# Kernel tuning notes

Hardware: AMD Instinct MI355X
Metric: run time of the kernel (lower is better)

Reference implementation:

```python
import jax, jax.numpy as jnp
import numpy as np
import math

S, B, D_MODEL = 1024, 2, 1024
N_HEADS = 16
D_HEAD = D_MODEL // N_HEADS
C = 32  # compressed_len


def _xavier(key, shape):
    fan_in, fan_out = shape[-1], shape[-2] if len(shape) > 1 else shape[-1]
    limit = math.sqrt(6.0 / (fan_in + fan_out))
    return jax.random.uniform(key, shape, jnp.float32, -limit, limit)


def setup_inputs() -> dict:
    key = jax.random.key(0)
    ks = jax.random.split(key, 10)
    return {
        "x": jax.random.normal(ks[0], (S, B, D_MODEL), jnp.float32),
        "q_down": _xavier(ks[1], (C, D_MODEL)),
        "Wq": _xavier(ks[2], (D_MODEL, D_MODEL)),
        "bq": jnp.zeros((D_MODEL,), jnp.float32),
        "Wk": _xavier(ks[3], (D_MODEL, D_MODEL)),
        "bk": jnp.zeros((D_MODEL,), jnp.float32),
        "Wv": _xavier(ks[4], (D_MODEL, D_MODEL)),
        "bv": jnp.zeros((D_MODEL,), jnp.float32),
        "Wo": _xavier(ks[5], (D_MODEL, D_MODEL)),
        "bo": jnp.zeros((D_MODEL,), jnp.float32),
    }


def reference(x, q_down, Wq, bq, Wk, bk, Wv, bv, Wo, bo):
    # x: (s, b, d_model); causal=True, rope=None, dropout inactive (eval)
    s, b, d_model = x.shape
    h, dh = N_HEADS, D_HEAD
    scale = 1.0 / math.sqrt(dh)

    q_u = x @ Wq.T + bq                       # (s,b,dm)
    k_d = x @ Wk.T + bk
    v_d = x @ Wv.T + bv
    v_d_k = v_d @ Wk.T + bk
    v_d_v = v_d @ Wv.T + bv

    def heads(t):  # (s,b,dm) -> (b,h,s,dh)
        return t.reshape(s, b, h, dh).transpose(1, 2, 0, 3)

    q_u = heads(q_u) * scale
    k_d = heads(k_d)
    v_d_kv = jnp.concatenate([heads(v_d_k), heads(v_d_v)], axis=-1)  # (b,h,s,2dh)

    q_d = q_down.reshape(C, h, dh).transpose(1, 0, 2) * scale        # (h,c,dh)

    down = jnp.einsum('hcd,bhsd->bhcs', q_d, k_d)                    # (b,h,c,s)
    w = jnp.exp(down - jnp.max(down, axis=-1, keepdims=True))
    norm = jnp.cumsum(w, axis=-1)

    # (b,h,c,s,2dh): running compressed KV state
    kv_u = jnp.cumsum(w[..., None] * v_d_kv[:, :, None, :, :], axis=3) / norm[..., None]
    k_u, v_u = jnp.split(kv_u, 2, axis=-1)                           # each (b,h,c,s,dh)

    up = jnp.einsum('bhsd,bhcsd->bhsc', q_u, k_u)
    up = jax.nn.softmax(up, axis=-1)
    out = jnp.einsum('bhsc,bhcsd->bhsd', up, v_u)                    # (b,h,s,dh)

    out = out.transpose(2, 0, 1, 3).reshape(s, b, d_model)
    return out @ Wo.T + bo
```

## Files before the change

kernel.cpp:

```cpp
#include <hip/hip_runtime.h>
#include <cstdint>
#include <cstddef>

#define S_LEN 1024
#define BATCH 2
#define DM    1024
#define NH    16
#define DH    64
#define CC    32
#define SB    2048
#define TSD   128
#define NCHD  8

using short8 = __attribute__((ext_vector_type(8))) short;
using f32x4  = __attribute__((ext_vector_type(4))) float;

__device__ __forceinline__ float b2f(unsigned short u) {
    union { unsigned int i; float f; } v; v.i = ((unsigned int)u) << 16; return v.f;
}
__device__ __forceinline__ unsigned short f2b(float f) {
    union { float f; unsigned int i; } v; v.f = f;
    unsigned int x = v.i;
    unsigned int r = x + 0x7FFFu + ((x >> 16) & 1u);
    return (unsigned short)(r >> 16);
}

__device__ __forceinline__ void async_ld16(const unsigned short* g, unsigned short* l) {
    __builtin_amdgcn_global_load_lds(
        (const __attribute__((address_space(1))) unsigned int*)g,
        (__attribute__((address_space(3))) unsigned int*)l,
        16, 0, 0);
}

__global__ __launch_bounds__(256) void k_convert(
    const void* x, const void* qd,
    const void* wq, const void* wk, const void* wv, const void* wo,
    const void* bq, const void* bk, const void* bv, const void* bo,
    int* __restrict__ flag,
    unsigned short* xb, unsigned short* qdb,
    unsigned short* Wqb, unsigned short* Wkb, unsigned short* Wvb, unsigned short* Wob,
    float* biasf)
{
    __shared__ int cnt;
    if (threadIdx.x == 0) cnt = 0;
    __syncthreads();
    {
        const unsigned short* xs = (const unsigned short*)x;
        int local = 0;
        for (int i = threadIdx.x; i < 1024; i += 256) {
            unsigned e = (xs[i * 2] >> 7) & 0xFF;
            if (e >= 90 && e <= 160) local++;
        }
        atomicAdd(&cnt, local);
    }
    __syncthreads();
    const int isbf = (cnt >= 640);
    if (blockIdx.x == 0 && threadIdx.x == 0) *flag = isbf;

    const size_t tid = (size_t)blockIdx.x * 256 + threadIdx.x;
    const size_t stride = (size_t)gridDim.x * 256;

    if (!isbf) {
        auto cv = [&](const void* src, unsigned short* dst, size_t n) {
            const float4* s = (const float4*)src;
            for (size_t i = tid; i < n / 4; i += stride) {
                float4 v = s[i];
                ushort4 o;
                o.x = f2b(v.x); o.y = f2b(v.y); o.z = f2b(v.z); o.w = f2b(v.w);
                ((ushort4*)dst)[i] = o;
            }
        };
        cv(x,  xb,  (size_t)SB * DM);
        cv(qd, qdb, (size_t)CC * DM);
        cv(wq, Wqb, (size_t)DM * DM);
        cv(wk, Wkb, (size_t)DM * DM);
        cv(wv, Wvb, (size_t)DM * DM);
        cv(wo, Wob, (size_t)DM * DM);
    }
    for (size_t i = tid; i < 5 * DM; i += stride) {
        int w = (int)(i >> 10), o = (int)(i & 1023);
        float val;
        if (w == 4) val = 0.f;
        else {
            const void* bp = (w == 0) ? bq : ((w == 1) ? bk : ((w == 2) ? bv : bo));
            val = isbf ? b2f(((const unsigned short*)bp)[o]) : ((const float*)bp)[o];
        }
        biasf[i] = val;
    }
}

__global__ __launch_bounds__(256) void k_prep(const unsigned short* __restrict__ Wv0,
                                              const unsigned short* __restrict__ Wv1,
                                              const unsigned short* __restrict__ Wk0,
                                              const unsigned short* __restrict__ Wk1,
                                              const int* __restrict__ flag,
                                              const float* __restrict__ biasf,
                                              unsigned short* __restrict__ WvT,
                                              float* __restrict__ b2k,
                                              float* __restrict__ b2v)
{
    const int isbf = *flag;
    const unsigned short* Wvb = isbf ? Wv1 : Wv0;
    const unsigned short* Wkb = isbf ? Wk1 : Wk0;
    const int t = threadIdx.x;
    if (blockIdx.x < 128) {
        const int r0 = (blockIdx.x & 7) * 128;
        const int c0 = (blockIdx.x >> 3) * 64;
        __shared__ unsigned short T[128 * 68];
        for (int u = t; u < 128 * 8; u += 256) {
            int r = u >> 3, cb = (u & 7) * 8;
            *(short8*)&T[r * 68 + cb] = *(const short8*)&Wvb[(size_t)(r0 + r) * DM + c0 + cb];
        }
        __syncthreads();
        for (int u = t; u < 64 * 16; u += 256) {
            int c = u >> 4, r8 = (u & 15) * 8;
            short8 o;
#pragma unroll
            for (int k = 0; k < 8; ++k) o[k] = T[(r8 + k) * 68 + c];
            *(short8*)&WvT[(size_t)(c0 + c) * DM + r0 + r8] = o;
        }
    } else {
        const int idx = blockIdx.x - 128;
        const int set = idx >> 5;
        const int bx = idx & 31;
        const unsigned short* W = set ? Wvb : Wkb;
        const float* bvf = biasf + 2048;
        const float* badd = set ? (biasf + 2048) : (biasf + 1024);
        float* out = set ? b2v : b2k;
        const int w = t >> 6, l = t & 63;
        const int gw = bx * 4 + w;
        for (int i = 0; i < 8; ++i) {
            int row = gw * 8 + i;
            const unsigned short* wr = &W[(size_t)row * DM + l * 16];
            short8 a = *(const short8*)wr;
            short8 b = *(const short8*)(wr + 8);
            float s = 0.f;
#pragma unroll
            for (int j = 0; j < 8; ++j) {
                s += b2f((unsigned short)a[j]) * bvf[l * 16 + j];
                s += b2f((unsigned short)b[j]) * bvf[l * 16 + 8 + j];
            }
#pragma unroll
            for (int m = 1; m < 64; m <<= 1) s += __shfl_xor(s, m);
            if (l == 0) out[row] = s + badd[row];
        }
    }
}

struct GArg {
    const unsigned short* A0;
    const unsigned short* A1;
    const unsigned short* B0;
    const unsigned short* B1;
    const float* bias;
    void* out;
    float scale;
    int mode;
};

__global__ __launch_bounds__(256) void gemm_bt(GArg g0, GArg g1, GArg g2, GArg g3,
                                               const int* __restrict__ flag,
                                               int M, int N, int K)
{
    GArg ga = (blockIdx.z == 0) ? g0 : (blockIdx.z == 1) ? g1 : (blockIdx.z == 2) ? g2 : g3;
    const int isbf = *flag;
    const unsigned short* Ap = isbf ? ga.A1 : ga.A0;
    const unsigned short* Bp = isbf ? ga.B1 : ga.B0;
    const int m0 = blockIdx.y * 128;
    const int n0 = blockIdx.x * 128;
    __shared__ __align__(16) unsigned short As[2][128 * 32];
    __shared__ __align__(16) unsigned short Bs[2][128 * 32];
    const int t = threadIdx.x;
    const int w = t >> 6, l = t & 63;
    const int wy = w >> 1, wx = w & 1;
    const int lr = l >> 2;
    const int lk = (l & 3) * 8;
    const int ln = l & 15;
    const int lq = l >> 4;

    f32x4 acc[4][4] = {};

    const unsigned short* Ab0 = Ap + (size_t)(m0 + w * 32 +      lr) * K + lk;
    const unsigned short* Ab1 = Ap + (size_t)(m0 + w * 32 + 16 + lr) * K + lk;
    const unsigned short* Bb0 = Bp + (size_t)(n0 + w * 32 +      lr) * K + lk;
    const unsigned short* Bb1 = Bp + (size_t)(n0 + w * 32 + 16 + lr) * K + lk;

    for (int kk = 0; kk < K; kk += 64) {
#pragma unroll
        for (int hh = 0; hh < 2; ++hh) {
            async_ld16(Ab0 + kk + hh * 32, &As[hh][w * 1024]);
            async_ld16(Ab1 + kk + hh * 32, &As[hh][w * 1024 + 512]);
            async_ld16(Bb0 + kk + hh * 32, &Bs[hh][w * 1024]);
            async_ld16(Bb1 + kk + hh * 32, &Bs[hh][w * 1024 + 512]);
        }
        __syncthreads();
#pragma unroll
        for (int hh = 0; hh < 2; ++hh) {
            short8 af[4], bfr[4];
#pragma unroll
            for (int i = 0; i < 4; ++i)
                af[i] = *(const short8*)&As[hh][(wy * 64 + i * 16 + ln) * 32 + lq * 8];
#pragma unroll
            for (int j = 0; j < 4; ++j)
                bfr[j] = *(const short8*)&Bs[hh][(wx * 64 + j * 16 + ln) * 32 + lq * 8];
#pragma unroll
            for (int i = 0; i < 4; ++i)
#pragma unroll
                for (int j = 0; j < 4; ++j)
                    acc[i][j] = __builtin_amdgcn_mfma_f32_16x16x32_bf16(af[i], bfr[j], acc[i][j], 0, 0, 0);
        }
        __syncthreads();
    }

    const int f32o = (ga.mode == 0) ? 1 : (ga.mode == 1) ? 0 : (!isbf);
    const float sc = ga.scale;
#pragma unroll
    for (int j = 0; j < 4; ++j) {
        int col = n0 + wx * 64 + j * 16 + ln;
        float bv = ga.bias[col];
#pragma unroll
        for (int i = 0; i < 4; ++i) {
            int row0 = m0 + wy * 64 + i * 16 + lq * 4;
#pragma unroll
            for (int r = 0; r < 4; ++r) {
                float v = (acc[i][j][r] + bv) * sc;
                size_t idx = (size_t)(row0 + r) * N + col;
                if (f32o) ((float*)ga.out)[idx] = v;
                else      ((unsigned short*)ga.out)[idx] = f2b(v);
            }
        }
    }
}

__global__ __launch_bounds__(256) void gemm_bt_n64(GArg g0, GArg g1,
                                                   const int* __restrict__ flag,
                                                   int M, int N, int K)
{
    GArg ga = (blockIdx.z == 0) ? g0 : g1;
    const int isbf = *flag;
    const unsigned short* Ap = isbf ? ga.A1 : ga.A0;
    const unsigned short* Bp = isbf ? ga.B1 : ga.B0;
    const int m0 = blockIdx.y * 128;
    const int n0 = blockIdx.x * 64;
    __shared__ __align__(16) unsigned short As[2][128 * 32];
    __shared__ __align__(16) unsigned short Bs[2][64 * 32];
    const int t = threadIdx.x;
    const int w = t >> 6, l = t & 63;
    const int wy = w >> 1, wx = w & 1;
    const int lr = l >> 2;
    const int lk = (l & 3) * 8;
    const int ln = l & 15;
    const int lq = l >> 4;

    f32x4 acc[4][2] = {};

    const unsigned short* Ab0 = Ap + (size_t)(m0 + w * 32 +      lr) * K + lk;
    const unsigned short* Ab1 = Ap + (size_t)(m0 + w * 32 + 16 + lr) * K + lk;
    const unsigned short* Bb  = Bp + (size_t)(n0 + w * 16 + lr) * K + lk;

    for (int kk = 0; kk < K; kk += 64) {
#pragma unroll
        for (int hh = 0; hh < 2; ++hh) {
            async_ld16(Ab0 + kk + hh * 32, &As[hh][w * 1024]);
            async_ld16(Ab1 + kk + hh * 32, &As[hh][w * 1024 + 512]);
            async_ld16(Bb  + kk + hh * 32, &Bs[hh][w * 512]);
        }
        __syncthreads();
#pragma unroll
        for (int hh = 0; hh < 2; ++hh) {
            short8 af[4], bfr[2];
#pragma unroll
            for (int i = 0; i < 4; ++i)
                af[i] = *(const short8*)&As[hh][(wy * 64 + i * 16 + ln) * 32 + lq * 8];
#pragma unroll
            for (int j = 0; j < 2; ++j)
                bfr[j] = *(const short8*)&Bs[hh][(wx * 32 + j * 16 + ln) * 32 + lq * 8];
#pragma unroll
            for (int i = 0; i < 4; ++i)
#pragma unroll
                for (int j = 0; j < 2; ++j)
                    acc[i][j] = __builtin_amdgcn_mfma_f32_16x16x32_bf16(af[i], bfr[j], acc[i][j], 0, 0, 0);
        }
        __syncthreads();
    }

    const int f32o = (ga.mode == 0) ? 1 : (ga.mode == 1) ? 0 : (!isbf);
    const float sc = ga.scale;
#pragma unroll
    for (int j = 0; j < 2; ++j) {
        int col = n0 + wx * 32 + j * 16 + ln;
        float bv = ga.bias[col];
#pragma unroll
        for (int i = 0; i < 4; ++i) {
            int row0 = m0 + wy * 64 + i * 16 + lq * 4;
#pragma unroll
            for (int r = 0; r < 4; ++r) {
                float v = (acc[i][j][r] + bv) * sc;
                size_t idx = (size_t)(row0 + r) * N + col;
                if (f32o) ((float*)ga.out)[idx] = v;
                else      ((unsigned short*)ga.out)[idx] = f2b(v);
            }
        }
    }
}

__global__ __launch_bounds__(256) void k_down(const unsigned short* __restrict__ kd,
                                              const unsigned short* __restrict__ qd0,
                                              const unsigned short* __restrict__ qd1,
                                              const int* __restrict__ flag,
                                              float* __restrict__ wbuf,
                                              float* __restrict__ cmax,
                                              float* __restrict__ csum)
{
    const unsigned short* qdw = (*flag) ? qd1 : qd0;
    const int bh = blockIdx.x;
    const int b = bh >> 4, h = bh & 15;
    const int chunk = blockIdx.y;
    const int s0 = chunk * TSD;
    const int t = threadIdx.x;
    const int w = t >> 6, l = t & 63;
    const int ln = l & 15, lq = l >> 4;

    __shared__ __align__(16) unsigned short QD[32 * 72];
    __shared__ __align__(16) unsigned short KT[128 * 72];
    __shared__ float SS[32 * 132];
    __shared__ float pm[256];
    __shared__ float cmf[CC];

    {
        int r = t >> 3, cb = (t & 7) * 8;
        *(short8*)&QD[r * 72 + cb] = *(const short8*)&qdw[(size_t)r * DM + h * DH + cb];
    }
    for (int u = t; u < 128 * 8; u += 256) {
        int r = u >> 3, cb = (u & 7) * 8;
        *(short8*)&KT[r * 72 + cb] =
            *(const short8*)&kd[(size_t)((s0 + r) * BATCH + b) * DM + h * DH + cb];
    }
    __syncthreads();

    f32x4 accG[2][2] = {};
#pragma unroll
    for (int ks = 0; ks < 2; ++ks) {
        short8 a8[2], b8[2];
#pragma unroll
        for (int i = 0; i < 2; ++i)
            a8[i] = *(const short8*)&QD[(i * 16 + ln) * 72 + ks * 32 + lq * 8];
#pragma unroll
        for (int j = 0; j < 2; ++j)
            b8[j] = *(const short8*)&KT[(w * 32 + j * 16 + ln) * 72 + ks * 32 + lq * 8];
#pragma unroll
        for (int i = 0; i < 2; ++i)
#pragma unroll
            for (int j = 0; j < 2; ++j)
                accG[i][j] = __builtin_amdgcn_mfma_f32_16x16x32_bf16(a8[i], b8[j], accG[i][j], 0, 0, 0);
    }
#pragma unroll
    for (int i = 0; i < 2; ++i) {
#pragma unroll
        for (int j = 0; j < 2; ++j) {
            int sl = w * 32 + j * 16 + ln;
#pragma unroll
            for (int r = 0; r < 4; ++r) {
                int c = i * 16 + lq * 4 + r;
                float v = accG[i][j][r] * 0.125f;
                SS[c * 132 + sl] = v;
                wbuf[((size_t)bh * CC + c) * S_LEN + s0 + sl] = v;
            }
        }
    }
    __syncthreads();

    const int c = t >> 3, sub = t & 7;
    float lmax = -3.4e38f;
#pragma unroll
    for (int k = 0; k < 16; ++k) lmax = fmaxf(lmax, SS[c * 132 + sub * 16 + k]);
    lmax = fmaxf(lmax, __shfl_xor(lmax, 1));
    lmax = fmaxf(lmax, __shfl_xor(lmax, 2));
    lmax = fmaxf(lmax, __shfl_xor(lmax, 4));
    if (sub == 0) {
        cmf[c] = lmax;
        cmax[((size_t)bh * CC + c) * NCHD + chunk] = lmax;
    }
    __syncthreads();
    const float cm = cmf[c];
    float es = 0.f;
#pragma unroll
    for (int k = 0; k < 16; ++k) es += __expf(SS[c * 132 + sub * 16 + k] - cm);
    es += __shfl_xor(es, 1);
    es += __shfl_xor(es, 2);
    es += __shfl_xor(es, 4);
    if (sub == 0) csum[((size_t)bh * CC + c) * NCHD + chunk] = es;
}

__global__ __launch_bounds__(256) void k_wapply(const float* __restrict__ wbuf,
                                                const float* __restrict__ cmax,
                                                const float* __restrict__ csum,
                                                unsigned short* __restrict__ wb,
                                                unsigned short* __restrict__ wT,
                                                float* __restrict__ invn)
{
    const int bh = blockIdx.x, seg = blockIdx.y;
    const int t = threadIdx.x;
    __shared__ float gm[CC];
    __shared__ float basep[CC];
    __shared__ float psum[CC][9];
    __shared__ unsigned short wTt[128 * 40];
    __shared__ float invt[128 * 36];

    if (t < CC) {
        const size_t cb = (size_t)(bh * CC + t) * NCHD;
        float m = cmax[cb];
#pragma unroll
        for (int g = 1; g < NCHD; ++g) m = fmaxf(m, cmax[cb + g]);
        gm[t] = m;
        float bsum = 0.f;
        for (int k = 0; k < seg; ++k)
            bsum += csum[cb + k] * __expf(cmax[cb + k] - m);
        basep[t] = bsum;
    }
    __syncthreads();

    const int c = t >> 3, sub = t & 7;
    const float gmc = gm[c];
    const size_t rbase = (size_t)bh * 32768 + c * 1024 + seg * 128 + sub * 16;
    float w16[16];
    float s = 0.f;
#pragma unroll
    for (int i = 0; i < 16; ++i) {
        float v = __expf(wbuf[rbase + i] - gmc);
        w16[i] = v; s += v;
    }
    psum[c][sub] = s;
    short8 o0, o1;
#pragma unroll
    for (int i = 0; i < 8; ++i) { o0[i] = f2b(w16[i]); o1[i] = f2b(w16[8 + i]); }
    *(short8*)&wb[rbase] = o0;
    *(short8*)&wb[rbase + 8] = o1;
#pragma unroll
    for (int i = 0; i < 16; ++i) wTt[(sub * 16 + i) * 40 + c] = f2b(w16[i]);
    __syncthreads();

    float run = basep[c];
    for (int k = 0; k < sub; ++k) run += psum[c][k];
#pragma unroll
    for (int i = 0; i < 16; ++i) {
        run += w16[i];
        invt[(sub * 16 + i) * 36 + c] = 1.0f / fmaxf(run, 1e-30f);
    }
    __syncthreads();

    for (int u = t; u < 128 * 4; u += 256) {
        int r = u >> 2, cb = (u & 3) * 8;
        *(short8*)&wT[(size_t)bh * 32768 + (seg * 128 + r) * 32 + cb] =
            *(const short8*)&wTt[r * 40 + cb];
    }
    for (int u = t; u < 128 * 8; u += 256) {
        int r = u >> 3, cb = (u & 7) * 4;
        *(float4*)&invn[(size_t)bh * 32768 + (seg * 128 + r) * 32 + cb] =
            *(const float4*)&invt[r * 36 + cb];
    }
}

__global__ __launch_bounds__(256) void k_state(const unsigned short* __restrict__ wb,
                                               const unsigned short* __restrict__ vdk,
                                               const unsigned short* __restrict__ vdv,
                                               float* __restrict__ Mst,
                                               float* __restrict__ NTst)
{
    const int bh = blockIdx.x, ch = blockIdx.y;
    const int b = bh >> 4, h = bh & 15;
    const int s0 = ch * 64;
    const int t = threadIdx.x;
    const int w = t >> 6, l = t & 63;
    const int ln = l & 15, lq = l >> 4;
    __shared__ __align__(16) unsigned short Ws[32 * 72];
    __shared__ __align__(16) unsigned short T1[64 * 72];
    __shared__ __align__(16) unsigned short T2[64 * 72];
    __shared__ __align__(16) unsigned short KT[64 * 72];
    __shared__ __align__(16) unsigned short VT[64 * 72];

    for (int u = t; u < 32 * 8; u += 256) {
        int r = u >> 3, cb = (u & 7) * 8;
        *(short8*)&Ws[r * 72 + cb] = *(const short8*)&wb[(size_t)bh * 32768 + r * 1024 + s0 + cb];
    }
    for (int u = t; u < 64 * 8; u += 256) {
        int r = u >> 3, cb = (u & 7) * 8;
        *(short8*)&T1[r * 72 + cb] =
            *(const short8*)&vdk[(size_t)((s0 + r) * BATCH + b) * DM + h * DH + cb];
        *(short8*)&T2[r * 72 + cb] =
            *(const short8*)&vdv[(size_t)((s0 + r) * BATCH + b) * DM + h * DH + cb];
    }
    __syncthreads();
    for (int u = t; u < 64 * 8; u += 256) {
        int d = u >> 3, s8 = (u & 7) * 8;
        short8 o1, o2;
#pragma unroll
        for (int k = 0; k < 8; ++k) {
            o1[k] = T1[(s8 + k) * 72 + d];
            o2[k] = T2[(s8 + k) * 72 + d];
        }
        *(short8*)&KT[d * 72 + s8] = o1;
        *(short8*)&VT[d * 72 + s8] = o2;
    }
    __syncthreads();

    f32x4 accM[2] = {};
#pragma unroll
    for (int ks = 0; ks < 2; ++ks) {
        short8 b8 = *(const short8*)&KT[(w * 16 + ln) * 72 + ks * 32 + lq * 8];
#pragma unroll
        for (int i = 0; i < 2; ++i) {
            short8 a8 = *(const short8*)&Ws[(i * 16 + ln) * 72 + ks * 32 + lq * 8];
            accM[i] = __builtin_amdgcn_mfma_f32_16x16x32_bf16(a8, b8, accM[i], 0, 0, 0);
        }
    }
#pragma unroll
    for (int i = 0; i < 2; ++i)
#pragma unroll
        for (int r = 0; r < 4; ++r)
            Mst[((size_t)(bh * 16 + ch) * 32 + i * 16 + lq * 4 + r) * 64 + w * 16 + ln] = accM[i][r];

    f32x4 accN[2] = {};
#pragma unroll
    for (int ks = 0; ks < 2; ++ks) {
        short8 a8 = *(const short8*)&VT[(w * 16 + ln) * 72 + ks * 32 + lq * 8];
#pragma unroll
        for (int j = 0; j < 2; ++j) {
            short8 b8 = *(const short8*)&Ws[(j * 16 + ln) * 72 + ks * 32 + lq * 8];
            accN[j] = __builtin_amdgcn_mfma_f32_16x16x32_bf16(a8, b8, accN[j], 0, 0, 0);
        }
    }
#pragma unroll
    for (int j = 0; j < 2; ++j)
#pragma unroll
        for (int r = 0; r < 4; ++r)
            NTst[((size_t)(bh * 16 + ch) * 64 + w * 16 + lq * 4 + r) * 32 + j * 16 + ln] = accN[j][r];
}

__global__ __launch_bounds__(256) void k_prefix(const float* __restrict__ Mst,
                                                const float* __restrict__ NTst,
                                                unsigned short* __restrict__ Mcum,
                                                unsigned short* __restrict__ NTcum)
{
    const int bh = blockIdx.x;
    const float* src = blockIdx.y ? NTst : Mst;
    unsigned short* dst = blockIdx.y ? NTcum : Mcum;
    const int e0 = threadIdx.x * 8;
    float run[8];
#pragma unroll
    for (int j = 0; j < 8; ++j) run[j] = 0.f;
    for (int ch = 0; ch < 16; ++ch) {
        size_t off = (size_t)(bh * 16 + ch) * 2048 + e0;
        short8 ob;
#pragma unroll
        for (int j = 0; j < 8; ++j) ob[j] = f2b(run[j]);
        *(short8*)&dst[off] = ob;
#pragma unroll
        for (int j = 0; j < 8; ++j) run[j] += src[off + j];
    }
}

__global__ __launch_bounds__(256) void k_att(
    const unsigned short* __restrict__ qu,
    const unsigned short* __restrict__ vdk,
    const unsigned short* __restrict__ wb,
    const float* __restrict__ invn,
    const unsigned short* __restrict__ wT,
    const unsigned short* __restrict__ vdv,
    const unsigned short* __restrict__ Mcum,
    const unsigned short* __restrict__ NTcum,
    unsigned short* __restrict__ attout)
{
    const int bh = blockIdx.x, b = bh >> 4, h = bh & 15;
    const int qi = blockIdx.y;
    const int s0 = qi * 64;
    const int t = threadIdx.x;
    const int w = t >> 6, l = t & 63;
    const int wy = w >> 1, wx = w & 1;
    const int ln = l & 15, lq = l >> 4;

    __shared__ __align__(16) unsigned short Qs[64 * 72];
    __shared__ __align__(16) unsigned short Gs[64 * 72];
    __shared__ __align__(16) unsigned short Kd[64 * 72];
    __shared__ __align__(16) unsigned short Wd[32 * 72];
    __shared__ __align__(16) unsigned short WTd[64 * 40];
    __shared__ __align__(16) unsigned short VTd[64 * 72];
    __shared__ __align__(16) unsigned short Mc[32 * 72];
    __shared__ __align__(16) unsigned short Nc[64 * 40];

    for (int u = t; u < 64 * 8; u += 256) {
        int r = u >> 3, cb = (u & 7) * 8;
        *(short8*)&Qs[r * 72 + cb] =
            *(const short8*)&qu[(size_t)(s0 + r) * 2048 + b * 1024 + h * 64 + cb];
        *(short8*)&Kd[r * 72 + cb] =
            *(const short8*)&vdk[(size_t)(s0 + r) * 2048 + b * 1024 + h * 64 + cb];
        *(short8*)&Gs[r * 72 + cb] =
            *(const short8*)&vdv[(size_t)(s0 + r) * 2048 + b * 1024 + h * 64 + cb];
    }
    for (int u = t; u < 32 * 8; u += 256) {
        int r = u >> 3, cb = (u & 7) * 8;
        *(short8*)&Wd[r * 72 + cb] =
            *(const short8*)&wb[(size_t)bh * 32768 + r * 1024 + s0 + cb];
        *(short8*)&Mc[r * 72 + cb] =
            *(const short8*)&Mcum[((size_t)(bh * 16 + qi) * 32 + r) * 64 + cb];
    }
    for (int u = t; u < 64 * 4; u += 256) {
        int r = u >> 2, cb = (u & 3) * 8;
        *(short8*)&WTd[r * 40 + cb] =
            *(const short8*)&wT[(size_t)bh * 32768 + (s0 + r) * 32 + cb];
        *(short8*)&Nc[r * 40 + cb] =
            *(const short8*)&NTcum[((size_t)(bh * 16 + qi) * 64 + r) * 32 + cb];
    }
    __syncthreads();

    for (int u = t; u < 64 * 8; u += 256) {
        int d = u >> 3, s8 = (u & 7) * 8;
        short8 o;
#pragma unroll
        for (int k = 0; k < 8; ++k) o[k] = Gs[(s8 + k) * 72 + d];
        *(short8*)&VTd[d * 72 + s8] = o;
    }
    __syncthreads();

    {
        f32x4 accG[2][2] = {};
#pragma unroll
        for (int ks = 0; ks < 2; ++ks) {
            short8 a8[2], b8[2];
#pragma unroll
            for (int i = 0; i < 2; ++i)
                a8[i] = *(const short8*)&Qs[(wy * 32 + i * 16 + ln) * 72 + ks * 32 + lq * 8];
#pragma unroll
            for (int j = 0; j < 2; ++j)
                b8[j] = *(const short8*)&Kd[(wx * 32 + j * 16 + ln) * 72 + ks * 32 + lq * 8];
#pragma unroll
            for (int i = 0; i < 2; ++i)
#pragma unroll
                for (int j = 0; j < 2; ++j)
                    accG[i][j] = __builtin_amdgcn_mfma_f32_16x16x32_bf16(a8[i], b8[j], accG[i][j], 0, 0, 0);
        }
        __syncthreads();
#pragma unroll
        for (int i = 0; i < 2; ++i) {
            int row = wy * 32 + i * 16 + lq * 4;
#pragma unroll
            for (int j = 0; j < 2; ++j) {
                int col = wx * 32 + j * 16 + ln;
#pragma unroll
                for (int r = 0; r < 4; ++r) {
                    float v = accG[i][j][r];
                    if (col > row + r) v = 0.f;
                    Gs[(row + r) * 72 + col] = f2b(v);
                }
            }
        }
    }
    __syncthreads();

    f32x4 accU[2] = {};
#pragma unroll
    for (int ks = 0; ks < 2; ++ks) {
        short8 ga = *(const short8*)&Gs[(w * 16 + ln) * 72 + ks * 32 + lq * 8];
        short8 qa = *(const short8*)&Qs[(w * 16 + ln) * 72 + ks * 32 + lq * 8];
#pragma unroll
        for (int j = 0; j < 2; ++j) {
            short8 wf = *(const short8*)&Wd[(j * 16 + ln) * 72 + ks * 32 + lq * 8];
            short8 mf = *(const short8*)&Mc[(j * 16 + ln) * 72 + ks * 32 + lq * 8];
            accU[j] = __builtin_amdgcn_mfma_f32_16x16x32_bf16(ga, wf, accU[j], 0, 0, 0);
            accU[j] = __builtin_amdgcn_mfma_f32_16x16x32_bf16(qa, mf, accU[j], 0, 0, 0);
        }
    }
    __syncthreads();

    {
        int rowl = w * 16 + lq * 4;
#pragma unroll
        for (int r = 0; r < 4; ++r) {
            int srow = s0 + rowl + r;
            float inv0 = invn[(size_t)bh * 32768 + srow * 32 + ln];
            float inv1 = invn[(size_t)bh * 32768 + srow * 32 + 16 + ln];
            float l0 = accU[0][r] * inv0;
            float l1 = accU[1][r] * inv1;
            float m = fmaxf(l0, l1);
#pragma unroll
            for (int msk = 1; msk < 16; msk <<= 1) m = fmaxf(m, __shfl_xor(m, msk));
            float e0 = __expf(l0 - m), e1 = __expf(l1 - m);
            float Z = e0 + e1;
#pragma unroll
            for (int msk = 1; msk < 16; msk <<= 1) Z += __shfl_xor(Z, msk);
            float iz = 1.0f / Z;
            Qs[(rowl + r) * 40 + ln]      = f2b(e0 * iz * inv0);
            Qs[(rowl + r) * 40 + 16 + ln] = f2b(e1 * iz * inv1);
        }
    }
    __syncthreads();

    short8 pa[2];
#pragma unroll
    for (int i = 0; i < 2; ++i)
        pa[i] = *(const short8*)&Qs[(wy * 32 + i * 16 + ln) * 40 + lq * 8];
    {
        f32x4 accS[2][2] = {};
        short8 b8[2];
#pragma unroll
        for (int j = 0; j < 2; ++j)
            b8[j] = *(const short8*)&WTd[(wx * 32 + j * 16 + ln) * 40 + lq * 8];
#pragma unroll
        for (int i = 0; i < 2; ++i)
#pragma unroll
            for (int j = 0; j < 2; ++j)
                accS[i][j] = __builtin_amdgcn_mfma_f32_16x16x32_bf16(pa[i], b8[j], accS[i][j], 0, 0, 0);
#pragma unroll
        for (int i = 0; i < 2; ++i) {
            int row = wy * 32 + i * 16 + lq * 4;
#pragma unroll
            for (int j = 0; j < 2; ++j) {
                int col = wx * 32 + j * 16 + ln;
#pragma unroll
                for (int r = 0; r < 4; ++r) {
                    float v = accS[i][j][r];
                    if (col > row + r) v = 0.f;
                    Gs[(row + r) * 72 + col] = f2b(v);
                }
            }
        }
    }
    __syncthreads();

    {
        f32x4 accO[2][2] = {};
        short8 n8[2];
#pragma unroll
        for (int j = 0; j < 2; ++j)
            n8[j] = *(const short8*)&Nc[(wx * 32 + j * 16 + ln) * 40 + lq * 8];
#pragma unroll
        for (int i = 0; i < 2; ++i)
#pragma unroll
            for (int j = 0; j < 2; ++j)
                accO[i][j] = __builtin_amdgcn_mfma_f32_16x16x32_bf16(pa[i], n8[j], accO[i][j], 0, 0, 0);
#pragma unroll
        for (int ks = 0; ks < 2; ++ks) {
            short8 a8[2], b8[2];
#pragma unroll
            for (int i = 0; i < 2; ++i)
                a8[i] = *(const short8*)&Gs[(wy * 32 + i * 16 + ln) * 72 + ks * 32 + lq * 8];
#pragma unroll
            for (int j = 0; j < 2; ++j)
                b8[j] = *(const short8*)&VTd[(wx * 32 + j * 16 + ln) * 72 + ks * 32 + lq * 8];
#pragma unroll
            for (int i = 0; i < 2; ++i)
#pragma unroll
                for (int j = 0; j < 2; ++j)
                    accO[i][j] = __builtin_amdgcn_mfma_f32_16x16x32_bf16(a8[i], b8[j], accO[i][j], 0, 0, 0);
        }
#pragma unroll
        for (int i = 0; i < 2; ++i) {
            int rowb = s0 + wy * 32 + i * 16 + lq * 4;
#pragma unroll
            for (int j = 0; j < 2; ++j) {
                int d = wx * 32 + j * 16 + ln;
#pragma unroll
                for (int r = 0; r < 4; ++r)
                    attout[(size_t)(rowb + r) * 2048 + b * 1024 + h * 64 + d] = f2b(accO[i][j][r]);
            }
        }
    }
}

extern "C" void kernel_launch(void* const* d_in, const int* in_sizes, int n_in,
                              void* d_out, int out_size, void* d_ws, size_t ws_size,
                              hipStream_t stream)
{
    (void)in_sizes; (void)n_in; (void)out_size; (void)ws_size;
    char* ws = (char*)d_ws;
    const size_t MB = (size_t)1 << 20;
    const size_t KB = (size_t)1 << 10;
    unsigned short* attout = (unsigned short*)(ws + 0 * MB);
    unsigned short* q_u    = (unsigned short*)(ws + 4 * MB);
    unsigned short* k_d    = (unsigned short*)(ws + 8 * MB);
    unsigned short* v_dk   = (unsigned short*)(ws + 12 * MB);
    unsigned short* v_dv   = (unsigned short*)(ws + 16 * MB);
    float* wbuf = (float*)(ws + 20 * MB);
    unsigned short* wb  = (unsigned short*)(ws + 24 * MB);
    unsigned short* wT  = (unsigned short*)(ws + 26 * MB);
    float* invn = (float*)(ws + 28 * MB);
    float* Mst  = (float*)(ws + 32 * MB);
    float* NTst = (float*)(ws + 36 * MB);
    unsigned short* Mcum  = (unsigned short*)(ws + 40 * MB);
    unsigned short* NTcum = (unsigned short*)(ws + 42 * MB);
    unsigned short* xb  = (unsigned short*)(ws + 44 * MB);
    unsigned short* Wqb = (unsigned short*)(ws + 48 * MB);
    unsigned short* Wkb = (unsigned short*)(ws + 50 * MB);
    unsigned short* Wvb = (unsigned short*)(ws + 52 * MB);
    unsigned short* Wob = (unsigned short*)(ws + 54 * MB);
    unsigned short* WvT = (unsigned short*)(ws + 56 * MB);
    unsigned short* W2k = (unsigned short*)(ws + 58 * MB);
    unsigned short* W2v = (unsigned short*)(ws + 60 * MB);
    unsigned short* qdb = (unsigned short*)(ws + 62 * MB);
    float* biasf  = (float*)(ws + 62 * MB + 64 * KB);
    float* b2k    = (float*)(ws + 62 * MB + 128 * KB);
    float* b2v    = (float*)(ws + 62 * MB + 132 * KB);
    float* cmax   = (float*)(ws + 62 * MB + 192 * KB);
    float* csum   = (float*)(ws + 62 * MB + 256 * KB);
    int*   flag   = (int*)  (ws + 62 * MB + 320 * KB);

    const unsigned short* xraw  = (const unsigned short*)d_in[0];
    const unsigned short* qdraw = (const unsigned short*)d_in[1];
    const unsigned short* wqraw = (const unsigned short*)d_in[2];
    const unsigned short* wkraw = (const unsigned short*)d_in[4];
    const unsigned short* wvraw = (const unsigned short*)d_in[6];
    const unsigned short* woraw = (const unsigned short*)d_in[8];

    k_convert<<<1024, 256, 0, stream>>>(
        d_in[0], d_in[1], d_in[2], d_in[4], d_in[6], d_in[8],
        d_in[3], d_in[5], d_in[7], d_in[9],
        flag, xb, qdb, Wqb, Wkb, Wvb, Wob, biasf);

    const float* bqf = biasf;
    const float* bkf = biasf + 1024;
    const float* bof = biasf + 3072;
    const float* zerof = biasf + 4096;

    k_prep<<<192, 256, 0, stream>>>(Wvb, wvraw, Wkb, wkraw, flag, biasf, WvT, b2k, b2v);
    GArg wpk{ Wkb, wkraw, WvT, WvT, zerof, (void*)W2k, 1.0f, 1 };
    GArg wpv{ Wvb, wvraw, WvT, WvT, zerof, (void*)W2v, 1.0f, 1 };
    gemm_bt_n64<<<dim3(16, 8, 2), 256, 0, stream>>>(wpk, wpv, flag, DM, DM, DM);

    GArg gq { xb, xraw, Wqb, wqraw, bqf, (void*)q_u, 0.125f, 1 };
    GArg gk { xb, xraw, Wkb, wkraw, bkf, (void*)k_d, 1.0f, 1 };
    GArg gvk{ xb, xraw, W2k, W2k,   b2k, (void*)v_dk, 1.0f, 1 };
    GArg gvv{ xb, xraw, W2v, W2v,   b2v, (void*)v_dv, 1.0f, 1 };
    gemm_bt<<<dim3(8, 16, 4), 256, 0, stream>>>(gq, gk, gvk, gvv, flag, SB, DM, DM);

    k_down<<<dim3(32, NCHD), 256, 0, stream>>>(k_d, qdb, qdraw, flag, wbuf, cmax, csum);
    k_wapply<<<dim3(32, 8), 256, 0, stream>>>(wbuf, cmax, csum, wb, wT, invn);
    k_state<<<dim3(32, 16), 256, 0, stream>>>(wb, v_dk, v_dv, Mst, NTst);
    k_prefix<<<dim3(32, 2), 256, 0, stream>>>(Mst, NTst, Mcum, NTcum);
    k_att<<<dim3(32, 16), 256, 0, stream>>>(q_u, v_dk, wb, invn, wT, v_dv, Mcum, NTcum, attout);

    GArg go{ attout, attout, Wob, woraw, bof, d_out, 1.0f, 2 };
    gemm_bt_n64<<<dim3(16, 16, 1), 256, 0, stream>>>(go, go, flag, SB, DM, DM);
}
```

Baseline: 192.7 us.

## Replace precomputed combined weights with two-stage V projection; widen prefix grid

Removes the weight-product precomputation (transpose of Wv, Wk·Wv and Wv·Wv GEMMs plus fused bias) and instead computes v_d = x·Wv^T first, then applies Wk and Wv to v_d in a second GEMM launch. This trades a 1024^3-sized weight GEMM pair plus a prep kernel for a serialized second activation GEMM over 2048 rows, and it rounds v_d to bf16 before the second projection. The prefix-sum kernel is also split across 4 z-blocks with 2 elements per thread, giving it more parallelism.

```diff
diff --git a/kernel.cpp b/kernel.cpp
--- a/kernel.cpp
+++ b/kernel.cpp
@@ -89,64 +89,6 @@
     }
 }
 
-__global__ __launch_bounds__(256) void k_prep(const unsigned short* __restrict__ Wv0,
-                                              const unsigned short* __restrict__ Wv1,
-                                              const unsigned short* __restrict__ Wk0,
-                                              const unsigned short* __restrict__ Wk1,
-                                              const int* __restrict__ flag,
-                                              const float* __restrict__ biasf,
-                                              unsigned short* __restrict__ WvT,
-                                              float* __restrict__ b2k,
-                                              float* __restrict__ b2v)
-{
-    const int isbf = *flag;
-    const unsigned short* Wvb = isbf ? Wv1 : Wv0;
-    const unsigned short* Wkb = isbf ? Wk1 : Wk0;
-    const int t = threadIdx.x;
-    if (blockIdx.x < 128) {
-        const int r0 = (blockIdx.x & 7) * 128;
-        const int c0 = (blockIdx.x >> 3) * 64;
-        __shared__ unsigned short T[128 * 68];
-        for (int u = t; u < 128 * 8; u += 256) {
-            int r = u >> 3, cb = (u & 7) * 8;
-            *(short8*)&T[r * 68 + cb] = *(const short8*)&Wvb[(size_t)(r0 + r) * DM + c0 + cb];
-        }
-        __syncthreads();
-        for (int u = t; u < 64 * 16; u += 256) {
-            int c = u >> 4, r8 = (u & 15) * 8;
-            short8 o;
-#pragma unroll
-            for (int k = 0; k < 8; ++k) o[k] = T[(r8 + k) * 68 + c];
-            *(short8*)&WvT[(size_t)(c0 + c) * DM + r0 + r8] = o;
-        }
-    } else {
-        const int idx = blockIdx.x - 128;
-        const int set = idx >> 5;
-        const int bx = idx & 31;
-        const unsigned short* W = set ? Wvb : Wkb;
-        const float* bvf = biasf + 2048;
-        const float* badd = set ? (biasf + 2048) : (biasf + 1024);
-        float* out = set ? b2v : b2k;
-        const int w = t >> 6, l = t & 63;
-        const int gw = bx * 4 + w;
-        for (int i = 0; i < 8; ++i) {
-            int row = gw * 8 + i;
-            const unsigned short* wr = &W[(size_t)row * DM + l * 16];
-            short8 a = *(const short8*)wr;
-            short8 b = *(const short8*)(wr + 8);
-            float s = 0.f;
-#pragma unroll
-            for (int j = 0; j < 8; ++j) {
-                s += b2f((unsigned short)a[j]) * bvf[l * 16 + j];
-                s += b2f((unsigned short)b[j]) * bvf[l * 16 + 8 + j];
-            }
-#pragma unroll
-            for (int m = 1; m < 64; m <<= 1) s += __shfl_xor(s, m);
-            if (l == 0) out[row] = s + badd[row];
-        }
-    }
-}
-
 struct GArg {
     const unsigned short* A0;
     const unsigned short* A1;
@@ -545,18 +487,15 @@
     const int bh = blockIdx.x;
     const float* src = blockIdx.y ? NTst : Mst;
     unsigned short* dst = blockIdx.y ? NTcum : Mcum;
-    const int e0 = threadIdx.x * 8;
-    float run[8];
-#pragma unroll
-    for (int j = 0; j < 8; ++j) run[j] = 0.f;
+    const int e0 = blockIdx.z * 512 + threadIdx.x * 2;
+    float r0 = 0.f, r1 = 0.f;
+#pragma unroll
     for (int ch = 0; ch < 16; ++ch) {
         size_t off = (size_t)(bh * 16 + ch) * 2048 + e0;
-        short8 ob;
-#pragma unroll
-        for (int j = 0; j < 8; ++j) ob[j] = f2b(run[j]);
-        *(short8*)&dst[off] = ob;
-#pragma unroll
-        for (int j = 0; j < 8; ++j) run[j] += src[off + j];
+        ushort2 ob; ob.x = f2b(r0); ob.y = f2b(r1);
+        *(ushort2*)&dst[off] = ob;
+        float2 v = *(const float2*)&src[off];
+        r0 += v.x; r1 += v.y;
     }
 }
 
@@ -793,13 +732,9 @@
     unsigned short* Wkb = (unsigned short*)(ws + 50 * MB);
     unsigned short* Wvb = (unsigned short*)(ws + 52 * MB);
     unsigned short* Wob = (unsigned short*)(ws + 54 * MB);
-    unsigned short* WvT = (unsigned short*)(ws + 56 * MB);
-    unsigned short* W2k = (unsigned short*)(ws + 58 * MB);
-    unsigned short* W2v = (unsigned short*)(ws + 60 * MB);
+    unsigned short* v_d = (unsigned short*)(ws + 56 * MB);
     unsigned short* qdb = (unsigned short*)(ws + 62 * MB);
     float* biasf  = (float*)(ws + 62 * MB + 64 * KB);
-    float* b2k    = (float*)(ws + 62 * MB + 128 * KB);
-    float* b2v    = (float*)(ws + 62 * MB + 132 * KB);
     float* cmax   = (float*)(ws + 62 * MB + 192 * KB);
     float* csum   = (float*)(ws + 62 * MB + 256 * KB);
     int*   flag   = (int*)  (ws + 62 * MB + 320 * KB);
@@ -818,24 +753,22 @@
 
     const float* bqf = biasf;
     const float* bkf = biasf + 1024;
+    const float* bvf = biasf + 2048;
     const float* bof = biasf + 3072;
-    const float* zerof = biasf + 4096;
-
-    k_prep<<<192, 256, 0, stream>>>(Wvb, wvraw, Wkb, wkraw, flag, biasf, WvT, b2k, b2v);
-    GArg wpk{ Wkb, wkraw, WvT, WvT, zerof, (void*)W2k, 1.0f, 1 };
-    GArg wpv{ Wvb, wvraw, WvT, WvT, zerof, (void*)W2v, 1.0f, 1 };
-    gemm_bt_n64<<<dim3(16, 8, 2), 256, 0, stream>>>(wpk, wpv, flag, DM, DM, DM);
 
     GArg gq { xb, xraw, Wqb, wqraw, bqf, (void*)q_u, 0.125f, 1 };
     GArg gk { xb, xraw, Wkb, wkraw, bkf, (void*)k_d, 1.0f, 1 };
-    GArg gvk{ xb, xraw, W2k, W2k,   b2k, (void*)v_dk, 1.0f, 1 };
-    GArg gvv{ xb, xraw, W2v, W2v,   b2v, (void*)v_dv, 1.0f, 1 };
-    gemm_bt<<<dim3(8, 16, 4), 256, 0, stream>>>(gq, gk, gvk, gvv, flag, SB, DM, DM);
+    GArg gv { xb, xraw, Wvb, wvraw, bvf, (void*)v_d, 1.0f, 1 };
+    gemm_bt<<<dim3(8, 16, 3), 256, 0, stream>>>(gq, gk, gv, gq, flag, SB, DM, DM);
+
+    GArg gvk{ v_d, v_d, Wkb, wkraw, bkf, (void*)v_dk, 1.0f, 1 };
+    GArg gvv{ v_d, v_d, Wvb, wvraw, bvf, (void*)v_dv, 1.0f, 1 };
+    gemm_bt<<<dim3(8, 16, 2), 256, 0, stream>>>(gvk, gvv, gvk, gvk, flag, SB, DM, DM);
 
     k_down<<<dim3(32, NCHD), 256, 0, stream>>>(k_d, qdb, qdraw, flag, wbuf, cmax, csum);
     k_wapply<<<dim3(32, 8), 256, 0, stream>>>(wbuf, cmax, csum, wb, wT, invn);
     k_state<<<dim3(32, 16), 256, 0, stream>>>(wb, v_dk, v_dv, Mst, NTst);
-    k_prefix<<<dim3(32, 2), 256, 0, stream>>>(Mst, NTst, Mcum, NTcum);
+    k_prefix<<<dim3(32, 2, 4), 256, 0, stream>>>(Mst, NTst, Mcum, NTcum);
     k_att<<<dim3(32, 16), 256, 0, stream>>>(q_u, v_dk, wb, invn, wT, v_dv, Mcum, NTcum, attout);
 
     GArg go{ attout, attout, Wob, woraw, bof, d_out, 1.0f, 2 };
```

Result: no change. 189.4 us (-1.7%).
